# Performance work log

Hardware: AMD Instinct MI355X
Metric: run time of the kernel (lower is better)

Reference implementation:

```python
import jax, jax.numpy as jnp
import numpy as np

NEG_SLOPE = 0.2  # PyG GATConv default leaky_relu slope
H1, F1 = 4, 64


def gat_layer(x, src, dst, n, W, a_src, a_dst, b, heads, out_dim, concat):
    # Linear transform then split heads: [N, H, F]
    h = (x @ W).reshape(n, heads, out_dim)
    # Per-node attention logits for source/destination roles: [N, H]
    e_src = jnp.sum(h * a_src, axis=-1)
    e_dst = jnp.sum(h * a_dst, axis=-1)
    # Per-edge score, LeakyReLU: [E, H]
    e = e_src[src] + e_dst[dst]
    e = jnp.where(e > 0, e, NEG_SLOPE * e)
    # Segment softmax over incoming edges of each destination node
    m = jax.ops.segment_max(e, dst, num_segments=n)  # [N, H]
    e = jnp.exp(e - jax.lax.stop_gradient(m)[dst])
    denom = jax.ops.segment_sum(e, dst, num_segments=n)  # [N, H]
    alpha = e / denom[dst]  # [E, H]
    # Scatter-aggregate weighted source features: [N, H, F]
    out = jax.ops.segment_sum(alpha[:, :, None] * h[src], dst, num_segments=n)
    if concat:
        out = out.reshape(n, heads * out_dim)
    else:
        out = out.mean(axis=1)
    return out + b


def setup_inputs() -> dict:
    key = jax.random.key(0)
    ks = jax.random.split(key, 16)
    N, E, D_IN, HID, C = 30000, 480000, 5000, 64, 3
    s = 0.05
    inp = {
        "x": jax.random.normal(ks[0], (N, D_IN), dtype=jnp.float32),
        "W1": jax.random.normal(ks[1], (D_IN, H1 * HID), dtype=jnp.float32) * s,
        "a1_src": jax.random.normal(ks[2], (H1, HID), dtype=jnp.float32) * s,
        "a1_dst": jax.random.normal(ks[3], (H1, HID), dtype=jnp.float32) * s,
        "b1": jnp.zeros((H1 * HID,), dtype=jnp.float32),
        "W2": jax.random.normal(ks[4], (H1 * HID, H1 * HID), dtype=jnp.float32) * s,
        "a2_src": jax.random.normal(ks[5], (H1, HID), dtype=jnp.float32) * s,
        "a2_dst": jax.random.normal(ks[6], (H1, HID), dtype=jnp.float32) * s,
        "b2": jnp.zeros((H1 * HID,), dtype=jnp.float32),
        "W3": jax.random.normal(ks[7], (H1 * HID, HID), dtype=jnp.float32) * s,
        "a3_src": jax.random.normal(ks[8], (1, HID), dtype=jnp.float32) * s,
        "a3_dst": jax.random.normal(ks[9], (1, HID), dtype=jnp.float32) * s,
        "b3": jnp.zeros((HID,), dtype=jnp.float32),
        "Wc": jax.random.normal(ks[10], (HID, C), dtype=jnp.float32) * s,
        "bc": jnp.zeros((C,), dtype=jnp.float32),
        "edge_index": jax.random.randint(ks[11], (2, E), 0, N, dtype=jnp.int64)
        if jax.config.jax_enable_x64
        else jax.random.randint(ks[11], (2, E), 0, N, dtype=jnp.int32),
    }
    return inp


def reference(x, W1, a1_src, a1_dst, b1, W2, a2_src, a2_dst, b2,
              W3, a3_src, a3_dst, b3, Wc, bc, edge_index):
    n = x.shape[0]
    loops = jnp.arange(n, dtype=edge_index.dtype)
    src = jnp.concatenate([edge_index[0], loops])  # add self-loops (PyG default)
    dst = jnp.concatenate([edge_index[1], loops])
    h = gat_layer(x, src, dst, n, W1, a1_src, a1_dst, b1, H1, F1, True)
    h = jax.nn.elu(h)
    h = gat_layer(h, src, dst, n, W2, a2_src, a2_dst, b2, H1, F1, True)
    h = jax.nn.elu(h)
    h = gat_layer(h, src, dst, n, W3, a3_src, a3_dst, b3, 1, F1, False)
    h = jax.nn.elu(h)
    return h @ Wc + bc
```

## Files before the change

kernel.cpp:

```cpp
#include <hip/hip_runtime.h>
#include <hip/hip_bf16.h>
#include <cstdint>
#include <cstddef>

typedef unsigned short u16;
typedef __attribute__((ext_vector_type(8))) short short8;
typedef __attribute__((ext_vector_type(4))) float f4;


__device__ __forceinline__ u16 f2bf(float x) {
    union { float f; uint32_t u; } v; v.f = x;
    uint32_t r = v.u + 0x7fffu + ((v.u >> 16) & 1u);
    return (u16)(r >> 16);
}

__device__ __forceinline__ void async16(const u16* g, u16* l) {
    __builtin_amdgcn_global_load_lds((__attribute__((address_space(1))) void*)(g),
                                     (__attribute__((address_space(3))) void*)(l),
                                     16, 0, 0);
}


template<int BM, int BN, int WM, int WN>
__global__ __launch_bounds__((BM/WM)*(BN/WN)*64)
void gemm_xw(const float* __restrict__ A, const u16* __restrict__ Bt,
             float* __restrict__ C, int M, int K, int KT)
{
    constexpr int WAVES   = (BM/WM)*(BN/WN);
    constexpr int THREADS = WAVES*64;
    constexpr int RF = WM/16, CF = WN/16;
    constexpr int BCH = (BN*64)/(16*THREADS);
    static_assert((BM*32)/THREADS == 8, "A staging assumes 8 floats per thread");

    __shared__ __align__(16) u16 As[BM*32];
    __shared__ __align__(16) u16 Bs[BN*32];

    const int tid  = threadIdx.x;
    const int wid  = tid >> 6, lane = tid & 63;
    const int quad = lane >> 4, l16 = lane & 15;
    constexpr int WCOLS = BN/WN;
    const int wm = (wid / WCOLS) * WM;
    const int wn = (wid % WCOLS) * WN;
    const long m0 = (long)blockIdx.x * BM;

    const int arow = tid >> 2;
    const int akk  = (tid & 3) * 8;
    const bool aok = (m0 + arow) < M;
    const float* aptr = A + (size_t)(m0 + arow) * K + akk;

    f4 acc[RF][CF];
    #pragma unroll
    for (int r = 0; r < RF; ++r)
        #pragma unroll
        for (int c = 0; c < CF; ++c)
            #pragma unroll
            for (int g = 0; g < 4; ++g) acc[r][c][g] = 0.f;

    const u16* Asl = As + (wm + l16)*32 + quad*8;
    const u16* Bsl = Bs + (wn + l16)*32 + quad*8;

    for (int kt = 0; kt < KT; ++kt) {
        __syncthreads();
        #pragma unroll
        for (int i = 0; i < BCH; ++i) {
            int c16 = i*THREADS + tid;
            async16(Bt + (size_t)kt*(BN*32) + (size_t)c16*8, (u16*)Bs + c16*8);
        }
        {
            const int gk = kt*32 + akk;
            f4 v0, v1;
            #pragma unroll
            for (int g = 0; g < 4; ++g) { v0[g] = 0.f; v1[g] = 0.f; }
            if (aok && gk < K) {
                const float* p = aptr + (size_t)kt*32;
                v0 = *(const f4*)p;
                v1 = *(const f4*)(p + 4);
            }
            short8 w;
            #pragma unroll
            for (int g = 0; g < 4; ++g) {
                w[g]   = (short)f2bf(v0[g]);
                w[4+g] = (short)f2bf(v1[g]);
            }
            *(short8*)(As + tid*8) = w;
        }
        __syncthreads();

        short8 af[RF], bfr[CF];
        #pragma unroll
        for (int r = 0; r < RF; ++r) af[r]  = *(const short8*)(Asl + r*16*32);
        #pragma unroll
        for (int c = 0; c < CF; ++c) bfr[c] = *(const short8*)(Bsl + c*16*32);
        #pragma unroll
        for (int r = 0; r < RF; ++r)
            #pragma unroll
            for (int c = 0; c < CF; ++c)
                acc[r][c] = __builtin_amdgcn_mfma_f32_16x16x32_bf16(af[r], bfr[c], acc[r][c], 0, 0, 0);
    }

    #pragma unroll
    for (int r = 0; r < RF; ++r) {
        const long rb = m0 + wm + r*16 + quad*4;
        #pragma unroll
        for (int c = 0; c < CF; ++c) {
            const int col = wn + c*16 + l16;
            #pragma unroll
            for (int g = 0; g < 4; ++g) {
                long row = rb + g;
                if (row < M) C[row*(long)BN + col] = acc[r][c][g];
            }
        }
    }
}

__global__ void k_prep_w(const float* __restrict__ W, u16* __restrict__ out,
                         int K, int Nn, int total)
{
    int idx = blockIdx.x*256 + threadIdx.x;
    if (idx >= total) return;
    int ki = idx & 31;
    int rest = idx >> 5;
    int nn = rest % Nn;
    int kt = rest / Nn;
    int k = kt*32 + ki;
    float v = (k < K) ? W[(size_t)k*Nn + nn] : 0.f;
    out[idx] = f2bf(v);
}

__global__ void k_hist(const int* __restrict__ ei, int E, int N, int* counts)
{
    int i = blockIdx.x*256 + threadIdx.x;
    if (i >= E + N) return;
    int d = (i < E) ? ei[E + i] : (i - E);
    atomicAdd(&counts[d], 1);
}

__global__ void k_scan1(const int* __restrict__ counts, int* offs, int* partials, int N)
{
    __shared__ int s[256];
    int i = blockIdx.x*256 + threadIdx.x;
    int v = (i < N) ? counts[i] : 0;
    s[threadIdx.x] = v;
    __syncthreads();
    #pragma unroll
    for (int off = 1; off < 256; off <<= 1) {
        int t = (threadIdx.x >= off) ? s[threadIdx.x - off] : 0;
        __syncthreads();
        s[threadIdx.x] += t;
        __syncthreads();
    }
    if (i < N) offs[i + 1] = s[threadIdx.x];
    if (threadIdx.x == 255) partials[blockIdx.x] = s[255];
    if (i == 0) offs[0] = 0;
}

__global__ void k_scan2(int* partials, int NB)
{
    __shared__ int s[256];
    int v = (threadIdx.x < NB) ? partials[threadIdx.x] : 0;
    s[threadIdx.x] = v;
    __syncthreads();
    for (int off = 1; off < 256; off <<= 1) {
        int t = (threadIdx.x >= off) ? s[threadIdx.x - off] : 0;
        __syncthreads();
        s[threadIdx.x] += t;
        __syncthreads();
    }
    if (threadIdx.x < NB) partials[threadIdx.x] = s[threadIdx.x] - v;
}

__global__ void k_scan3(int* offs, const int* __restrict__ partials, int N)
{
    int i = blockIdx.x*256 + threadIdx.x;
    if (i < N) offs[i + 1] += partials[blockIdx.x];
}

__global__ void k_copy(const int* __restrict__ a, int* __restrict__ b, int n)
{
    int i = blockIdx.x*256 + threadIdx.x;
    if (i < n) b[i] = a[i];
}

__global__ void k_scatter(const int* __restrict__ ei, int E, int N,
                          int* cursor, int* __restrict__ ssrc)
{
    int i = blockIdx.x*256 + threadIdx.x;
    if (i >= E + N) return;
    int s, d;
    if (i < E) { s = ei[i]; d = ei[E + i]; } else { s = i - E; d = s; }
    int pos = atomicAdd(&cursor[d], 1);
    ssrc[pos] = s;
}

__global__ void k_scores(const float* __restrict__ h, const float* __restrict__ asrc,
                         const float* __restrict__ adst, float* __restrict__ es,
                         float* __restrict__ ed, int N, int H)
{
    int wave = threadIdx.x >> 6, lane = threadIdx.x & 63;
    int node = blockIdx.x*4 + wave;
    if (node >= N) return;
    const float* row = h + (size_t)node * H * 64;
    for (int hh = 0; hh < H; ++hh) {
        float v = row[hh*64 + lane];
        float s = v * asrc[hh*64 + lane];
        float d = v * adst[hh*64 + lane];
        #pragma unroll
        for (int off = 32; off > 0; off >>= 1) {
            s += __shfl_down(s, off);
            d += __shfl_down(d, off);
        }
        if (lane == 0) { es[node*H + hh] = s; ed[node*H + hh] = d; }
    }
}

__global__ void k_stats(const int* __restrict__ offs, const int* __restrict__ ssrc,
                        const float* __restrict__ es, const float* __restrict__ ed,
                        float* __restrict__ mt, float* __restrict__ dt, int N, int H)
{
    int idx = blockIdx.x*blockDim.x + threadIdx.x;
    if (idx >= N*H) return;
    int n = idx / H, hh = idx - n*H;
    int s0 = offs[n], s1 = offs[n + 1];
    float edv = ed[idx];
    float mx = -1e30f;
    for (int j = s0; j < s1; ++j) {
        float e = es[ssrc[j]*H + hh] + edv;
        e = (e > 0.f) ? e : 0.2f*e;
        mx = fmaxf(mx, e);
    }
    float sum = 0.f;
    for (int j = s0; j < s1; ++j) {
        float e = es[ssrc[j]*H + hh] + edv;
        e = (e > 0.f) ? e : 0.2f*e;
        sum += __expf(e - mx);
    }
    mt[idx] = mx; dt[idx] = sum;
}

__global__ void k_agg(const float* __restrict__ h, const int* __restrict__ offs,
                      const int* __restrict__ ssrc, const float* __restrict__ es,
                      const float* __restrict__ ed, const float* __restrict__ mt,
                      const float* __restrict__ dt, const float* __restrict__ bias,
                      float* __restrict__ out, int N, int H)
{
    int n = blockIdx.x;
    int hh = threadIdx.x >> 6, lane = threadIdx.x & 63;
    int s0 = offs[n], s1 = offs[n + 1];
    int idx = n*H + hh;
    float edv = ed[idx], mx = mt[idx], rden = 1.0f / dt[idx];
    float acc = 0.f;
    const int stride = H*64;
    for (int j = s0; j < s1; ++j) {
        int sidx = ssrc[j];
        float e = es[sidx*H + hh] + edv;
        e = (e > 0.f) ? e : 0.2f*e;
        float alpha = __expf(e - mx) * rden;
        acc += alpha * h[(size_t)sidx*stride + hh*64 + lane];
    }
    float v = acc + bias[hh*64 + lane];
    out[(size_t)n*stride + hh*64 + lane] = (v > 0.f) ? v : (__expf(v) - 1.f);
}

__global__ void k_classifier(const float* __restrict__ h, const float* __restrict__ Wc,
                             const float* __restrict__ bc, float* __restrict__ out, int N)
{
    __shared__ float wc[192];
    __shared__ float bcs[3];
    if (threadIdx.x < 192) wc[threadIdx.x] = Wc[threadIdx.x];
    if (threadIdx.x < 3)   bcs[threadIdx.x] = bc[threadIdx.x];
    __syncthreads();
    int n = blockIdx.x*blockDim.x + threadIdx.x;
    if (n >= N) return;
    const float4* row = (const float4*)(h + (size_t)n*64);
    float a0 = 0.f, a1 = 0.f, a2 = 0.f;
    #pragma unroll
    for (int q = 0; q < 16; ++q) {
        float4 v = row[q];
        const float* w = &wc[q*12];
        a0 += v.x*w[0] + v.y*w[3] + v.z*w[6] + v.w*w[9];
        a1 += v.x*w[1] + v.y*w[4] + v.z*w[7] + v.w*w[10];
        a2 += v.x*w[2] + v.y*w[5] + v.z*w[8] + v.w*w[11];
    }
    out[n*3 + 0] = a0 + bcs[0];
    out[n*3 + 1] = a1 + bcs[1];
    out[n*3 + 2] = a2 + bcs[2];
}

extern "C" void kernel_launch(void* const* d_in, const int* in_sizes, int n_in,
                              void* d_out, int out_size, void* d_ws, size_t ws_size,
                              hipStream_t stream)
{
    const float* x   = (const float*)d_in[0];
    const float* W1  = (const float*)d_in[1];
    const float* a1s = (const float*)d_in[2];
    const float* a1d = (const float*)d_in[3];
    const float* b1  = (const float*)d_in[4];
    const float* W2  = (const float*)d_in[5];
    const float* a2s = (const float*)d_in[6];
    const float* a2d = (const float*)d_in[7];
    const float* b2  = (const float*)d_in[8];
    const float* W3  = (const float*)d_in[9];
    const float* a3s = (const float*)d_in[10];
    const float* a3d = (const float*)d_in[11];
    const float* b3  = (const float*)d_in[12];
    const float* Wc  = (const float*)d_in[13];
    const float* bc  = (const float*)d_in[14];
    const int*   ei  = (const int*)d_in[15];
    float* out = (float*)d_out;

    const int DIN = in_sizes[1] / 256;
    const int N   = in_sizes[0] / DIN;
    const int E   = in_sizes[15] / 2;
    const int KT1 = (DIN + 31) / 32;
    const int ET  = E + N;

    char* ws = (char*)d_ws;
    size_t off = 0;
    auto alloc = [&](size_t bytes) -> void* {
        void* p = ws + off;
        off += (bytes + 255) & ~(size_t)255;
        return p;
    };

    float* bufA   = (float*)alloc((size_t)N*256*4);
    float* bufB   = (float*)alloc((size_t)N*256*4);
    u16*  Wt1     = (u16*)alloc((size_t)KT1*256*32*2);
    u16*  Wt2     = (u16*)alloc((size_t)8*256*32*2);
    u16*  Wt3     = (u16*)alloc((size_t)8*64*32*2);
    float* es     = (float*)alloc((size_t)N*4*4);
    float* ed     = (float*)alloc((size_t)N*4*4);
    float* mt     = (float*)alloc((size_t)N*4*4);
    float* dt     = (float*)alloc((size_t)N*4*4);
    int* counts   = (int*)alloc((size_t)N*4);
    int* offs     = (int*)alloc((size_t)(N+1)*4);
    int* cursor   = (int*)alloc((size_t)N*4);
    int* partials = (int*)alloc(1024);
    int* ssrc     = (int*)alloc((size_t)ET*4);

    const int NB = (N + 255)/256;
    const int GM = (N + 63)/64;

    hipMemsetAsync(counts, 0, (size_t)N*4, stream);
    k_hist   <<<(ET+255)/256, 256, 0, stream>>>(ei, E, N, counts);
    k_scan1  <<<NB, 256, 0, stream>>>(counts, offs, partials, N);
    k_scan2  <<<1, 256, 0, stream>>>(partials, NB);
    k_scan3  <<<NB, 256, 0, stream>>>(offs, partials, N);
    k_copy   <<<NB, 256, 0, stream>>>(offs, cursor, N);
    k_scatter<<<(ET+255)/256, 256, 0, stream>>>(ei, E, N, cursor, ssrc);

    k_prep_w<<<(KT1*256*32+255)/256, 256, 0, stream>>>(W1, Wt1, DIN, 256, KT1*256*32);
    k_prep_w<<<(8*256*32+255)/256, 256, 0, stream>>>(W2, Wt2, 256, 256, 8*256*32);
    k_prep_w<<<(8*64*32+255)/256, 256, 0, stream>>>(W3, Wt3, 256, 64, 8*64*32);

    gemm_xw<64,256,64,64><<<GM, 256, 0, stream>>>(x, Wt1, bufA, N, DIN, KT1);
    k_scores<<<(N+3)/4, 256, 0, stream>>>(bufA, a1s, a1d, es, ed, N, 4);
    k_stats <<<(N*4+255)/256, 256, 0, stream>>>(offs, ssrc, es, ed, mt, dt, N, 4);
    k_agg   <<<N, 256, 0, stream>>>(bufA, offs, ssrc, es, ed, mt, dt, b1, bufB, N, 4);
    gemm_xw<64,256,64,64><<<GM, 256, 0, stream>>>(bufB, Wt2, bufA, N, 256, 8);
    k_scores<<<(N+3)/4, 256, 0, stream>>>(bufA, a2s, a2d, es, ed, N, 4);
    k_stats <<<(N*4+255)/256, 256, 0, stream>>>(offs, ssrc, es, ed, mt, dt, N, 4);
    k_agg   <<<N, 256, 0, stream>>>(bufA, offs, ssrc, es, ed, mt, dt, b2, bufB, N, 4);
    gemm_xw<64,64,16,64><<<GM, 256, 0, stream>>>(bufB, Wt3, bufA, N, 256, 8);
    k_scores<<<(N+3)/4, 256, 0, stream>>>(bufA, a3s, a3d, es, ed, N, 1);
    k_stats <<<(N+255)/256, 256, 0, stream>>>(offs, ssrc, es, ed, mt, dt, N, 1);
    k_agg   <<<N, 64, 0, stream>>>(bufA, offs, ssrc, es, ed, mt, dt, b3, bufB, N, 1);
    k_classifier<<<(N+255)/256, 256, 0, stream>>>(bufB, Wc, bc, out, N);
}
```

Before: 1.324 ms.

## Split-K first GEMM with fused reduce+scores, online softmax in aggregation

```diff
diff --git a/kernel.cpp b/kernel.cpp
--- a/kernel.cpp
+++ b/kernel.cpp
@@ -24,7 +24,7 @@
 template<int BM, int BN, int WM, int WN>
 __global__ __launch_bounds__((BM/WM)*(BN/WN)*64)
 void gemm_xw(const float* __restrict__ A, const u16* __restrict__ Bt,
-             float* __restrict__ C, int M, int K, int KT)
+             float* __restrict__ C, int M, int K, int KT, int ktPer)
 {
     constexpr int WAVES   = (BM/WM)*(BN/WN);
     constexpr int THREADS = WAVES*64;
@@ -43,6 +43,10 @@
     const int wn = (wid % WCOLS) * WN;
     const long m0 = (long)blockIdx.x * BM;
 
+    const int ktA = blockIdx.y * ktPer;
+    const int ktB = min(ktA + ktPer, KT);
+    float* Cp = C + (size_t)blockIdx.y * (size_t)M * BN;
+
     const int arow = tid >> 2;
     const int akk  = (tid & 3) * 8;
     const bool aok = (m0 + arow) < M;
@@ -59,7 +63,7 @@
     const u16* Asl = As + (wm + l16)*32 + quad*8;
     const u16* Bsl = Bs + (wn + l16)*32 + quad*8;
 
-    for (int kt = 0; kt < KT; ++kt) {
+    for (int kt = ktA; kt < ktB; ++kt) {
         __syncthreads();
         #pragma unroll
         for (int i = 0; i < BCH; ++i) {
@@ -107,10 +111,45 @@
             #pragma unroll
             for (int g = 0; g < 4; ++g) {
                 long row = rb + g;
-                if (row < M) C[row*(long)BN + col] = acc[r][c][g];
+                if (row < M) Cp[row*(long)BN + col] = acc[r][c][g];
             }
         }
     }
+}
+
+__global__ void k_reduce_scores(const float* __restrict__ parts, size_t partStride, int S,
+                                const float* __restrict__ asrc, const float* __restrict__ adst,
+                                float* __restrict__ h, float* __restrict__ es,
+                                float* __restrict__ ed, int N)
+{
+    int wave = threadIdx.x >> 6, lane = threadIdx.x & 63;
+    int node = blockIdx.x*4 + wave;
+    if (node >= N) return;
+    size_t base = (size_t)node*256 + lane*4;
+    f4 v;
+    #pragma unroll
+    for (int g = 0; g < 4; ++g) v[g] = 0.f;
+    for (int s = 0; s < S; ++s) {
+        f4 p = *(const f4*)(parts + s*partStride + base);
+        #pragma unroll
+        for (int g = 0; g < 4; ++g) v[g] += p[g];
+    }
+    *(f4*)(h + base) = v;
+
+    int hh = lane >> 4;
+    int c0 = (lane & 15) * 4;
+    float s = 0.f, d = 0.f;
+    #pragma unroll
+    for (int g = 0; g < 4; ++g) {
+        s += v[g] * asrc[hh*64 + c0 + g];
+        d += v[g] * adst[hh*64 + c0 + g];
+    }
+    #pragma unroll
+    for (int off = 1; off < 16; off <<= 1) {
+        s += __shfl_xor(s, off);
+        d += __shfl_xor(d, off);
+    }
+    if ((lane & 15) == 0) { es[node*4 + hh] = s; ed[node*4 + hh] = d; }
 }
 
 __global__ void k_prep_w(const float* __restrict__ W, u16* __restrict__ out,
@@ -213,51 +252,30 @@
     }
 }
 
-__global__ void k_stats(const int* __restrict__ offs, const int* __restrict__ ssrc,
-                        const float* __restrict__ es, const float* __restrict__ ed,
-                        float* __restrict__ mt, float* __restrict__ dt, int N, int H)
-{
-    int idx = blockIdx.x*blockDim.x + threadIdx.x;
-    if (idx >= N*H) return;
-    int n = idx / H, hh = idx - n*H;
-    int s0 = offs[n], s1 = offs[n + 1];
-    float edv = ed[idx];
-    float mx = -1e30f;
-    for (int j = s0; j < s1; ++j) {
-        float e = es[ssrc[j]*H + hh] + edv;
-        e = (e > 0.f) ? e : 0.2f*e;
-        mx = fmaxf(mx, e);
-    }
-    float sum = 0.f;
-    for (int j = s0; j < s1; ++j) {
-        float e = es[ssrc[j]*H + hh] + edv;
-        e = (e > 0.f) ? e : 0.2f*e;
-        sum += __expf(e - mx);
-    }
-    mt[idx] = mx; dt[idx] = sum;
-}
-
 __global__ void k_agg(const float* __restrict__ h, const int* __restrict__ offs,
                       const int* __restrict__ ssrc, const float* __restrict__ es,
-                      const float* __restrict__ ed, const float* __restrict__ mt,
-                      const float* __restrict__ dt, const float* __restrict__ bias,
+                      const float* __restrict__ ed, const float* __restrict__ bias,
                       float* __restrict__ out, int N, int H)
 {
     int n = blockIdx.x;
     int hh = threadIdx.x >> 6, lane = threadIdx.x & 63;
     int s0 = offs[n], s1 = offs[n + 1];
-    int idx = n*H + hh;
-    float edv = ed[idx], mx = mt[idx], rden = 1.0f / dt[idx];
-    float acc = 0.f;
+    float edv = ed[n*H + hh];
+    float m = -1e30f, l = 0.f, acc = 0.f;
     const int stride = H*64;
     for (int j = s0; j < s1; ++j) {
         int sidx = ssrc[j];
         float e = es[sidx*H + hh] + edv;
         e = (e > 0.f) ? e : 0.2f*e;
-        float alpha = __expf(e - mx) * rden;
-        acc += alpha * h[(size_t)sidx*stride + hh*64 + lane];
-    }
-    float v = acc + bias[hh*64 + lane];
+        if (e > m) {
+            float sc = __expf(m - e);
+            l *= sc; acc *= sc; m = e;
+        }
+        float p = __expf(e - m);
+        l += p;
+        acc += p * h[(size_t)sidx*stride + hh*64 + lane];
+    }
+    float v = acc / l + bias[hh*64 + lane];
     out[(size_t)n*stride + hh*64 + lane] = (v > 0.f) ? v : (__expf(v) - 1.f);
 }
 
@@ -313,6 +331,8 @@
     const int E   = in_sizes[15] / 2;
     const int KT1 = (DIN + 31) / 32;
     const int ET  = E + N;
+    const int SPLITS = 4;
+    const int KTP = (KT1 + SPLITS - 1) / SPLITS;
 
     char* ws = (char*)d_ws;
     size_t off = 0;
@@ -324,13 +344,12 @@
 
     float* bufA   = (float*)alloc((size_t)N*256*4);
     float* bufB   = (float*)alloc((size_t)N*256*4);
+    float* bufP   = (float*)alloc((size_t)SPLITS*N*256*4);
     u16*  Wt1     = (u16*)alloc((size_t)KT1*256*32*2);
     u16*  Wt2     = (u16*)alloc((size_t)8*256*32*2);
     u16*  Wt3     = (u16*)alloc((size_t)8*64*32*2);
     float* es     = (float*)alloc((size_t)N*4*4);
     float* ed     = (float*)alloc((size_t)N*4*4);
-    float* mt     = (float*)alloc((size_t)N*4*4);
-    float* dt     = (float*)alloc((size_t)N*4*4);
     int* counts   = (int*)alloc((size_t)N*4);
     int* offs     = (int*)alloc((size_t)(N+1)*4);
     int* cursor   = (int*)alloc((size_t)N*4);
@@ -352,17 +371,15 @@
     k_prep_w<<<(8*256*32+255)/256, 256, 0, stream>>>(W2, Wt2, 256, 256, 8*256*32);
     k_prep_w<<<(8*64*32+255)/256, 256, 0, stream>>>(W3, Wt3, 256, 64, 8*64*32);
 
-    gemm_xw<64,256,64,64><<<GM, 256, 0, stream>>>(x, Wt1, bufA, N, DIN, KT1);
-    k_scores<<<(N+3)/4, 256, 0, stream>>>(bufA, a1s, a1d, es, ed, N, 4);
-    k_stats <<<(N*4+255)/256, 256, 0, stream>>>(offs, ssrc, es, ed, mt, dt, N, 4);
-    k_agg   <<<N, 256, 0, stream>>>(bufA, offs, ssrc, es, ed, mt, dt, b1, bufB, N, 4);
-    gemm_xw<64,256,64,64><<<GM, 256, 0, stream>>>(bufB, Wt2, bufA, N, 256, 8);
+    gemm_xw<64,256,64,64><<<dim3(GM, SPLITS), 256, 0, stream>>>(x, Wt1, bufP, N, DIN, KT1, KTP);
+    k_reduce_scores<<<(N+3)/4, 256, 0, stream>>>(bufP, (size_t)N*256, SPLITS, a1s, a1d,
+                                                 bufA, es, ed, N);
+    k_agg   <<<N, 256, 0, stream>>>(bufA, offs, ssrc, es, ed, b1, bufB, N, 4);
+    gemm_xw<64,256,64,64><<<dim3(GM, 1), 256, 0, stream>>>(bufB, Wt2, bufA, N, 256, 8, 8);
     k_scores<<<(N+3)/4, 256, 0, stream>>>(bufA, a2s, a2d, es, ed, N, 4);
-    k_stats <<<(N*4+255)/256, 256, 0, stream>>>(offs, ssrc, es, ed, mt, dt, N, 4);
-    k_agg   <<<N, 256, 0, stream>>>(bufA, offs, ssrc, es, ed, mt, dt, b2, bufB, N, 4);
-    gemm_xw<64,64,16,64><<<GM, 256, 0, stream>>>(bufB, Wt3, bufA, N, 256, 8);
+    k_agg   <<<N, 256, 0, stream>>>(bufA, offs, ssrc, es, ed, b2, bufB, N, 4);
+    gemm_xw<64,64,16,64><<<dim3(GM, 1), 256, 0, stream>>>(bufB, Wt3, bufA, N, 256, 8, 8);
     k_scores<<<(N+3)/4, 256, 0, stream>>>(bufA, a3s, a3d, es, ed, N, 1);
-    k_stats <<<(N+255)/256, 256, 0, stream>>>(offs, ssrc, es, ed, mt, dt, N, 1);
-    k_agg   <<<N, 64, 0, stream>>>(bufA, offs, ssrc, es, ed, mt, dt, b3, bufB, N, 1);
+    k_agg   <<<N, 64, 0, stream>>>(bufA, offs, ssrc, es, ed, b3, bufB, N, 1);
     k_classifier<<<(N+255)/256, 256, 0, stream>>>(bufB, Wc, bc, out, N);
 }
```

Result: no change. 1.315 ms (-0.7%).
